# Kernel optimization log

Measured on AMD Instinct MI355X. Metric: run time of the kernel, lower is better.

## Reference

```python
import jax, jax.numpy as jnp
import numpy as np

B, NUM_OBJ, R, D, C = 1024, 128, 32, 512, 7  # scans, obj slots, rel samples, feat dim, rel classes
N = NUM_OBJ + R  # 160 graph nodes per scan


def setup_inputs() -> dict:
    key = jax.random.key(0)
    ks = jax.random.split(key, 8)
    obj_feats = jax.random.normal(ks[0], (B, NUM_OBJ, D), jnp.float32)
    pairs = jax.random.randint(ks[1], (B, R, 2), 0, NUM_OBJ, dtype=jnp.int32)
    init = lambda k, shape, fan_in: jax.random.normal(k, shape, jnp.float32) / np.float32(np.sqrt(fan_in))
    return {
        "obj_feats": obj_feats,
        "pairs": pairs,
        "fuse_w": init(ks[2], (2 * D, D), 2 * D), "fuse_b": jnp.zeros((D,), jnp.float32),
        "gcn_w": init(ks[3], (D, D), D), "gcn_b": jnp.zeros((D,), jnp.float32),
        "fc1_w": init(ks[4], (D, 256), D), "fc1_b": jnp.zeros((256,), jnp.float32),
        "fc2_w": init(ks[5], (256, 128), 256), "fc2_b": jnp.zeros((128,), jnp.float32),
        "fc3_w": init(ks[6], (128, C), 128), "fc3_b": jnp.zeros((C,), jnp.float32),
    }


def reference(obj_feats, pairs, fuse_w, fuse_b, gcn_w, gcn_b,
              fc1_w, fc1_b, fc2_w, fc2_b, fc3_w, fc3_b):
    # --- init_rel_node (pos_fuse=False): fuse sub/obj features per sampled pair ---
    sub = jnp.take_along_axis(obj_feats, pairs[:, :, 0:1], axis=1)  # [B,R,D]
    obj = jnp.take_along_axis(obj_feats, pairs[:, :, 1:2], axis=1)  # [B,R,D]
    init_rel = jnp.concatenate([sub, obj], axis=-1) @ fuse_w + fuse_b  # [B,R,D]

    # --- X: object node feats in rows [0,NUM_OBJ), rel node feats in rows [NUM_OBJ,N) ---
    X = jnp.concatenate([obj_feats, init_rel], axis=1)  # [B,N,D]

    # --- A: get_graph_gcn_with_rel -- scatter 4 directed edges per pair ---
    b_idx = jnp.arange(B)[:, None]                      # [B,1]
    ridx = NUM_OBJ + jnp.arange(R)[None, :]             # [1,R] rel node index j+num_obj
    p0, p1 = pairs[:, :, 0], pairs[:, :, 1]             # [B,R]
    A = jnp.zeros((B, N, N), jnp.float32)
    A = A.at[b_idx, p0, ridx].set(1.0)
    A = A.at[b_idx, ridx, p1].set(1.0)
    A = A.at[b_idx, p1, ridx].set(1.0)
    A = A.at[b_idx, ridx, p0].set(1.0)

    # --- simpleGCN: relu((A @ X) W + b) ---
    H = jax.nn.relu(jnp.einsum('bnm,bmd->bnd', A, X) @ gcn_w + gcn_b)  # [B,N,D]

    # --- residual: GCN rel-node output + init rel feats ---
    rel_feat = H[:, NUM_OBJ:, :] + init_rel  # [B,R,D]

    # --- proxi_detector (dropout = identity, eval behavior) ---
    h = jax.nn.relu(rel_feat @ fc1_w + fc1_b)
    h = jax.nn.relu(h @ fc2_w + fc2_b)
    logits = h @ fc3_w + fc3_b  # [B,R,C]
    return jax.nn.softmax(logits, axis=-1)
```

## Files before the change

### kernel.cpp

```cpp
#include <hip/hip_runtime.h>
#include <hip/hip_bf16.h>

#define B_    1024
#define NOBJ  128
#define RREL  32
#define DIM   512
#define MTOT  32768

typedef __bf16 bf16x8 __attribute__((ext_vector_type(8)));
typedef float  f32x4  __attribute__((ext_vector_type(4)));
typedef unsigned short us;

__device__ __forceinline__ us f2bf(float f) {
    unsigned int u = __float_as_uint(f);
    u += 0x7FFFu + ((u >> 16) & 1u);
    return (us)(u >> 16);
}
__device__ __forceinline__ float bf2f(us h) {
    return __uint_as_float(((unsigned int)h) << 16);
}

__device__ __forceinline__ void load16_to_lds(const us* g, us* l) {
    __builtin_amdgcn_global_load_lds((const __attribute__((address_space(1))) void*)g,
                                     (__attribute__((address_space(3))) void*)l,
                                     16, 0, 0);
}

__global__ __launch_bounds__(256) void gather_kernel(
        const float* __restrict__ obj, const int* __restrict__ pairs,
        us* __restrict__ As, us* __restrict__ Msum) {
    int t = threadIdx.x;
    int g = t >> 7;
    int c = t & 127;
    int base = blockIdx.x * 8;
#pragma unroll
    for (int rr = 0; rr < 4; ++rr) {
        int m  = base + rr * 2 + g;
        int b  = m >> 5;
        int p0 = pairs[(m << 1) + 0];
        int p1 = pairs[(m << 1) + 1];
        const float4* srow = (const float4*)(obj + (size_t)(b * NOBJ + p0) * DIM);
        const float4* orow = (const float4*)(obj + (size_t)(b * NOBJ + p1) * DIM);
        float4 s4 = srow[c];
        float4 o4 = orow[c];
        size_t arow = (size_t)m * 1024;
        ushort4 sb = make_ushort4(f2bf(s4.x), f2bf(s4.y), f2bf(s4.z), f2bf(s4.w));
        ushort4 ob = make_ushort4(f2bf(o4.x), f2bf(o4.y), f2bf(o4.z), f2bf(o4.w));
        *(ushort4*)(As + arow + c * 4)       = sb;
        *(ushort4*)(As + arow + 512 + c * 4) = ob;
        float4 mz = s4;
        if (p0 != p1) { mz.x += o4.x; mz.y += o4.y; mz.z += o4.z; mz.w += o4.w; }
        *(ushort4*)(Msum + (size_t)m * 512 + c * 4) =
            make_ushort4(f2bf(mz.x), f2bf(mz.y), f2bf(mz.z), f2bf(mz.w));
    }
}

__global__ __launch_bounds__(256) void prep_weights(
        const float* __restrict__ fw, const float* __restrict__ gw,
        const float* __restrict__ w1, const float* __restrict__ w2,
        us* __restrict__ WfT, us* __restrict__ WgT,
        us* __restrict__ W1T, us* __restrict__ W2T) {
    __shared__ float t32[32][33];
    int id = blockIdx.x;
    const float* in; us* out; int K, N, local;
    if (id < 512)      { in = fw; out = WfT; K = 1024; N = 512; local = id; }
    else if (id < 768) { in = gw; out = WgT; K = 512;  N = 512; local = id - 512; }
    else if (id < 896) { in = w1; out = W1T; K = 512;  N = 256; local = id - 768; }
    else               { in = w2; out = W2T; K = 256;  N = 128; local = id - 896; }
    int tilesN = N >> 5;
    int bk = (local / tilesN) * 32;
    int bn = (local % tilesN) * 32;
    int t  = threadIdx.x;
    int tx = t & 31, ty = t >> 5;
#pragma unroll
    for (int i = 0; i < 4; ++i)
        t32[ty + i * 8][tx] = in[(size_t)(bk + ty + i * 8) * N + bn + tx];
    __syncthreads();
#pragma unroll
    for (int i = 0; i < 4; ++i)
        out[(size_t)(bn + ty + i * 8) * K + bk + tx] = f2bf(t32[tx][ty + i * 8]);
}

__global__ __launch_bounds__(256, 2) void gemm_fused12(
        const us* __restrict__ As,
        const us* __restrict__ Msum,
        const us* __restrict__ WfT,
        const us* __restrict__ WgT,
        const float* __restrict__ fuse_b, const float* __restrict__ gcn_b,
        us* __restrict__ rf) {
    __shared__ __align__(16) us ldsA[128 * 32];
    __shared__ __align__(16) us ldsB[128 * 32];

    int tid  = threadIdx.x;
    int wid  = tid >> 6;
    int lane = tid & 63;
    int wm   = wid & 1;
    int wn   = wid >> 1;
    int m0   = blockIdx.x * 128;
    int n0   = blockIdx.y * 128;

    f32x4 accF[4][4], accG[4][4];
#pragma unroll
    for (int i = 0; i < 4; ++i)
#pragma unroll
        for (int j = 0; j < 4; ++j)
#pragma unroll
            for (int k = 0; k < 4; ++k) { accF[i][j][k] = 0.0f; accG[i][j][k] = 0.0f; }

    int r = tid >> 2, c = tid & 3;
    us* la0 = ldsA + wid * 512;
    us* la1 = ldsA + 2048 + wid * 512;
    us* lb0 = ldsB + wid * 512;
    us* lb1 = ldsB + 2048 + wid * 512;

    int arow = wm * 64 + (lane & 15);
    int brow = wn * 64 + (lane & 15);
    int koff = (lane >> 4) * 8;

    {
        const us* ag0 = As + (size_t)(m0 + r)      * 1024 + c * 8;
        const us* ag1 = As + (size_t)(m0 + 64 + r) * 1024 + c * 8;
        const us* bg0 = WfT + (size_t)(n0 + r)      * 1024 + c * 8;
        const us* bg1 = WfT + (size_t)(n0 + 64 + r) * 1024 + c * 8;
        for (int k0 = 0; k0 < 1024; k0 += 32) {
            __syncthreads();
            load16_to_lds(ag0 + k0, la0);
            load16_to_lds(ag1 + k0, la1);
            load16_to_lds(bg0 + k0, lb0);
            load16_to_lds(bg1 + k0, lb1);
            __syncthreads();
            bf16x8 a[4], b[4];
#pragma unroll
            for (int i = 0; i < 4; ++i)
                a[i] = *(const bf16x8*)(ldsA + (arow + i * 16) * 32 + koff);
#pragma unroll
            for (int j = 0; j < 4; ++j)
                b[j] = *(const bf16x8*)(ldsB + (brow + j * 16) * 32 + koff);
#pragma unroll
            for (int i = 0; i < 4; ++i)
#pragma unroll
                for (int j = 0; j < 4; ++j)
                    accF[i][j] = __builtin_amdgcn_mfma_f32_16x16x32_bf16(a[i], b[j], accF[i][j], 0, 0, 0);
        }
    }
    {
        const us* ag0 = Msum + (size_t)(m0 + r)      * 512 + c * 8;
        const us* ag1 = Msum + (size_t)(m0 + 64 + r) * 512 + c * 8;
        const us* bg0 = WgT + (size_t)(n0 + r)      * 512 + c * 8;
        const us* bg1 = WgT + (size_t)(n0 + 64 + r) * 512 + c * 8;
        for (int k0 = 0; k0 < 512; k0 += 32) {
            __syncthreads();
            load16_to_lds(ag0 + k0, la0);
            load16_to_lds(ag1 + k0, la1);
            load16_to_lds(bg0 + k0, lb0);
            load16_to_lds(bg1 + k0, lb1);
            __syncthreads();
            bf16x8 a[4], b[4];
#pragma unroll
            for (int i = 0; i < 4; ++i)
                a[i] = *(const bf16x8*)(ldsA + (arow + i * 16) * 32 + koff);
#pragma unroll
            for (int j = 0; j < 4; ++j)
                b[j] = *(const bf16x8*)(ldsB + (brow + j * 16) * 32 + koff);
#pragma unroll
            for (int i = 0; i < 4; ++i)
#pragma unroll
                for (int j = 0; j < 4; ++j)
                    accG[i][j] = __builtin_amdgcn_mfma_f32_16x16x32_bf16(a[i], b[j], accG[i][j], 0, 0, 0);
        }
    }

    int crow  = wm * 64 + (lane >> 4) * 4;
    int ccol0 = wn * 64 + (lane & 15);
    float bf_[4], bg_[4];
#pragma unroll
    for (int j = 0; j < 4; ++j) {
        bf_[j] = fuse_b[n0 + ccol0 + j * 16];
        bg_[j] = gcn_b [n0 + ccol0 + j * 16];
    }
#pragma unroll
    for (int i = 0; i < 4; ++i)
#pragma unroll
        for (int j = 0; j < 4; ++j) {
            int col = n0 + ccol0 + j * 16;
#pragma unroll
            for (int jj = 0; jj < 4; ++jj) {
                int row = m0 + crow + i * 16 + jj;
                float v = fmaxf(accG[i][j][jj] + bg_[j], 0.0f) + accF[i][j][jj] + bf_[j];
                rf[(size_t)row * 512 + col] = f2bf(v);
            }
        }
}

#define H1S 264
#define H2S 136
__global__ __launch_bounds__(256, 2) void tail_kernel(
        const us* __restrict__ rf,
        const us* __restrict__ W1T,
        const us* __restrict__ W2T,
        const float* __restrict__ b1, const float* __restrict__ b2,
        const float* __restrict__ w3, const float* __restrict__ b3,
        float* __restrict__ out) {
    __shared__ __align__(16) unsigned char pool[57888];
    us*    sA   = (us*)(pool);
    us*    sB   = (us*)(pool + 4096);
    us*    sH2  = (us*)(pool);
    us*    sH1  = (us*)(pool + 20480);
    float* sRed = (float*)(pool + 20480);
    float* sW3  = (float*)(pool + 54272);
    float* sB3  = (float*)(pool + 57856);

    int tid  = threadIdx.x;
    int wid  = tid >> 6;
    int lane = tid & 63;
    int m0   = blockIdx.x * 64;

    for (int i = tid; i < 128 * 7; i += 256) sW3[i] = w3[i];
    if (tid < 7) sB3[tid] = b3[tid];

    int r = tid >> 2, c = tid & 3;
    int koff = (lane >> 4) * 8;
    int l15  = lane & 15;

    f32x4 acc1[4][4];
#pragma unroll
    for (int i = 0; i < 4; ++i)
#pragma unroll
        for (int j = 0; j < 4; ++j)
#pragma unroll
            for (int k = 0; k < 4; ++k) acc1[i][j][k] = 0.0f;

    {
        const us* ag = rf + (size_t)(m0 + r) * 512 + c * 8;
        us* la = sA + wid * 512;
        for (int k0 = 0; k0 < 512; k0 += 32) {
            __syncthreads();
            load16_to_lds(ag + k0, la);
#pragma unroll
            for (int q = 0; q < 4; ++q)
                load16_to_lds(W1T + (size_t)(q * 64 + r) * 512 + k0 + c * 8,
                              sB + q * 2048 + wid * 512);
            __syncthreads();
            bf16x8 a[4], b[4];
#pragma unroll
            for (int i = 0; i < 4; ++i)
                a[i] = *(const bf16x8*)(sA + (l15 + i * 16) * 32 + koff);
#pragma unroll
            for (int j = 0; j < 4; ++j)
                b[j] = *(const bf16x8*)(sB + (wid * 64 + j * 16 + l15) * 32 + koff);
#pragma unroll
            for (int i = 0; i < 4; ++i)
#pragma unroll
                for (int j = 0; j < 4; ++j)
                    acc1[i][j] = __builtin_amdgcn_mfma_f32_16x16x32_bf16(a[i], b[j], acc1[i][j], 0, 0, 0);
        }
    }
#pragma unroll
    for (int i = 0; i < 4; ++i)
#pragma unroll
        for (int j = 0; j < 4; ++j) {
            int col = wid * 64 + j * 16 + l15;
            float bb = b1[col];
#pragma unroll
            for (int jj = 0; jj < 4; ++jj) {
                int row = i * 16 + (lane >> 4) * 4 + jj;
                sH1[row * H1S + col] = f2bf(fmaxf(acc1[i][j][jj] + bb, 0.0f));
            }
        }

    int nw = wid & 1, kw = wid >> 1;
    f32x4 acc2[4][4];
#pragma unroll
    for (int i = 0; i < 4; ++i)
#pragma unroll
        for (int j = 0; j < 4; ++j)
#pragma unroll
            for (int k = 0; k < 4; ++k) acc2[i][j][k] = 0.0f;

    for (int t = 0; t < 4; ++t) {
        __syncthreads();
#pragma unroll
        for (int s = 0; s < 2; ++s)
#pragma unroll
            for (int q = 0; q < 2; ++q)
                load16_to_lds(W2T + (size_t)(q * 64 + r) * 256 + s * 128 + t * 32 + c * 8,
                              sB + s * 4096 + q * 2048 + wid * 512);
        __syncthreads();
        bf16x8 a[4], b[4];
#pragma unroll
        for (int i = 0; i < 4; ++i)
            a[i] = *(const bf16x8*)(sH1 + (l15 + i * 16) * H1S + kw * 128 + t * 32 + koff);
#pragma unroll
        for (int j = 0; j < 4; ++j)
            b[j] = *(const bf16x8*)(sB + kw * 4096 + (nw * 64 + j * 16 + l15) * 32 + koff);
#pragma unroll
        for (int i = 0; i < 4; ++i)
#pragma unroll
            for (int j = 0; j < 4; ++j)
                acc2[i][j] = __builtin_amdgcn_mfma_f32_16x16x32_bf16(a[i], b[j], acc2[i][j], 0, 0, 0);
    }
    __syncthreads();
    if (kw == 1) {
#pragma unroll
        for (int i = 0; i < 4; ++i)
#pragma unroll
            for (int j = 0; j < 4; ++j) {
                int col = nw * 64 + j * 16 + l15;
#pragma unroll
                for (int jj = 0; jj < 4; ++jj) {
                    int row = i * 16 + (lane >> 4) * 4 + jj;
                    sRed[row * 132 + col] = acc2[i][j][jj];
                }
            }
    }
    __syncthreads();
    if (kw == 0) {
#pragma unroll
        for (int i = 0; i < 4; ++i)
#pragma unroll
            for (int j = 0; j < 4; ++j) {
                int col = nw * 64 + j * 16 + l15;
                float bb = b2[col];
#pragma unroll
                for (int jj = 0; jj < 4; ++jj) {
                    int row = i * 16 + (lane >> 4) * 4 + jj;
                    float v = acc2[i][j][jj] + sRed[row * 132 + col] + bb;
                    sH2[row * H2S + col] = f2bf(fmaxf(v, 0.0f));
                }
            }
    }
    __syncthreads();

    int row = tid >> 2;
    int p   = tid & 3;
    float accv[7];
#pragma unroll
    for (int cc = 0; cc < 7; ++cc) accv[cc] = 0.0f;
    const us* hrow = sH2 + row * H2S + p * 32;
    for (int kk = 0; kk < 8; ++kk) {
        ushort4 u = *(const ushort4*)(hrow + kk * 4);
        float f0 = bf2f(u.x), f1 = bf2f(u.y), f2 = bf2f(u.z), f3 = bf2f(u.w);
        int k = p * 32 + kk * 4;
#pragma unroll
        for (int cc = 0; cc < 7; ++cc) {
            accv[cc] = fmaf(f0, sW3[(k + 0) * 7 + cc], accv[cc]);
            accv[cc] = fmaf(f1, sW3[(k + 1) * 7 + cc], accv[cc]);
            accv[cc] = fmaf(f2, sW3[(k + 2) * 7 + cc], accv[cc]);
            accv[cc] = fmaf(f3, sW3[(k + 3) * 7 + cc], accv[cc]);
        }
    }
#pragma unroll
    for (int cc = 0; cc < 7; ++cc) {
        accv[cc] += __shfl_xor(accv[cc], 1);
        accv[cc] += __shfl_xor(accv[cc], 2);
    }
    if (p == 0) {
        float mx = accv[0] + sB3[0];
        float lg[7];
#pragma unroll
        for (int cc = 0; cc < 7; ++cc) { lg[cc] = accv[cc] + sB3[cc]; mx = fmaxf(mx, lg[cc]); }
        float sum = 0.f;
#pragma unroll
        for (int cc = 0; cc < 7; ++cc) { lg[cc] = __expf(lg[cc] - mx); sum += lg[cc]; }
        float inv = 1.0f / sum;
#pragma unroll
        for (int cc = 0; cc < 7; ++cc) out[(size_t)(m0 + row) * 7 + cc] = lg[cc] * inv;
    }
}

extern "C" void kernel_launch(void* const* d_in, const int* in_sizes, int n_in,
                              void* d_out, int out_size, void* d_ws, size_t ws_size,
                              hipStream_t stream) {
    (void)in_sizes; (void)n_in; (void)out_size; (void)ws_size;
    const float* obj    = (const float*)d_in[0];
    const int*   pairs  = (const int*)  d_in[1];
    const float* fuse_w = (const float*)d_in[2];
    const float* fuse_b = (const float*)d_in[3];
    const float* gcn_w  = (const float*)d_in[4];
    const float* gcn_b  = (const float*)d_in[5];
    const float* fc1_w  = (const float*)d_in[6];
    const float* fc1_b  = (const float*)d_in[7];
    const float* fc2_w  = (const float*)d_in[8];
    const float* fc2_b  = (const float*)d_in[9];
    const float* fc3_w  = (const float*)d_in[10];
    const float* fc3_b  = (const float*)d_in[11];
    float* out = (float*)d_out;

    char* ws = (char*)d_ws;
    us* As   = (us*)(ws);
    us* Msum = (us*)(ws + (64u  << 20));
    us* rf   = (us*)(ws + (96u  << 20));
    us* WfT  = (us*)(ws + (128u << 20));
    us* WgT  = (us*)(ws + (129u << 20));
    us* W1T  = (us*)(ws + (130u << 20));
    us* W2T  = (us*)(ws + (131u << 20));

    gather_kernel<<<MTOT / 8, 256, 0, stream>>>(obj, pairs, As, Msum);
    prep_weights<<<928, 256, 0, stream>>>(fuse_w, gcn_w, fc1_w, fc2_w,
                                          WfT, WgT, W1T, W2T);

    gemm_fused12<<<dim3(MTOT / 128, 4), 256, 0, stream>>>(
        As, Msum, WfT, WgT, fuse_b, gcn_b, rf);

    tail_kernel<<<MTOT / 64, 256, 0, stream>>>(
        rf, W1T, W2T, fc1_b, fc2_b, fc3_w, fc3_b, out);
}
```

Baseline: 449.6 us.

## Widen fused GEMM to full N with double-buffered LDS and single accumulator

The fused GEMM now uses 512-thread blocks that each cover all 512 output columns for 128 rows, instead of a 4-way grid split over N. This lets the A tile be loaded once per block rather than four times. Global-to-LDS loads are double-buffered, so the next K-slice is staged while MFMAs run on the current one, which cuts the syncs per step to one. The GCN result is computed first, ReLU'd in place, and then the fuse GEMM accumulates into the same registers, so one accumulator set replaces two. The trade-off is 64 KB+ of LDS per block and fewer blocks (256) on a large-CU GPU, which may reduce occupancy and parallelism.

Result: no change. 444.5 us (-1.1%).

```diff
diff --git a/kernel.cpp b/kernel.cpp
--- a/kernel.cpp
+++ b/kernel.cpp
@@ -81,113 +81,114 @@
         out[(size_t)(bn + ty + i * 8) * K + bk + tx] = f2bf(t32[tx][ty + i * 8]);
 }
 
-__global__ __launch_bounds__(256, 2) void gemm_fused12(
+__global__ __launch_bounds__(512, 2) void gemm_fused12(
         const us* __restrict__ As,
         const us* __restrict__ Msum,
         const us* __restrict__ WfT,
         const us* __restrict__ WgT,
         const float* __restrict__ fuse_b, const float* __restrict__ gcn_b,
         us* __restrict__ rf) {
-    __shared__ __align__(16) us ldsA[128 * 32];
-    __shared__ __align__(16) us ldsB[128 * 32];
+    __shared__ __align__(16) us ldsA[2][4096];
+    __shared__ __align__(16) us ldsB[2][16384];
 
     int tid  = threadIdx.x;
     int wid  = tid >> 6;
     int lane = tid & 63;
-    int wm   = wid & 1;
-    int wn   = wid >> 1;
+    int wm   = wid >> 2;
+    int wn   = wid & 3;
     int m0   = blockIdx.x * 128;
-    int n0   = blockIdx.y * 128;
-
-    f32x4 accF[4][4], accG[4][4];
-#pragma unroll
-    for (int i = 0; i < 4; ++i)
-#pragma unroll
-        for (int j = 0; j < 4; ++j)
-#pragma unroll
-            for (int k = 0; k < 4; ++k) { accF[i][j][k] = 0.0f; accG[i][j][k] = 0.0f; }
+
+    f32x4 acc[4][8];
+#pragma unroll
+    for (int i = 0; i < 4; ++i)
+#pragma unroll
+        for (int j = 0; j < 8; ++j)
+#pragma unroll
+            for (int k = 0; k < 4; ++k) acc[i][j][k] = 0.0f;
 
     int r = tid >> 2, c = tid & 3;
-    us* la0 = ldsA + wid * 512;
-    us* la1 = ldsA + 2048 + wid * 512;
-    us* lb0 = ldsB + wid * 512;
-    us* lb1 = ldsB + 2048 + wid * 512;
-
-    int arow = wm * 64 + (lane & 15);
-    int brow = wn * 64 + (lane & 15);
+    const us* aG = Msum + (size_t)(m0 + r) * 512  + c * 8;
+    const us* aF = As   + (size_t)(m0 + r) * 1024 + c * 8;
+
+    int l15  = lane & 15;
     int koff = (lane >> 4) * 8;
-
-    {
-        const us* ag0 = As + (size_t)(m0 + r)      * 1024 + c * 8;
-        const us* ag1 = As + (size_t)(m0 + 64 + r) * 1024 + c * 8;
-        const us* bg0 = WfT + (size_t)(n0 + r)      * 1024 + c * 8;
-        const us* bg1 = WfT + (size_t)(n0 + 64 + r) * 1024 + c * 8;
-        for (int k0 = 0; k0 < 1024; k0 += 32) {
-            __syncthreads();
-            load16_to_lds(ag0 + k0, la0);
-            load16_to_lds(ag1 + k0, la1);
-            load16_to_lds(bg0 + k0, lb0);
-            load16_to_lds(bg1 + k0, lb1);
-            __syncthreads();
-            bf16x8 a[4], b[4];
+    int aoff = (wm * 64  + l15) * 32 + koff;
+    int boff = (wn * 128 + l15) * 32 + koff;
+
+    float bg_[8], bf_[8];
+#pragma unroll
+    for (int j = 0; j < 8; ++j) {
+        int col = wn * 128 + j * 16 + l15;
+        bg_[j] = gcn_b[col];
+        bf_[j] = fuse_b[col];
+    }
+
+    auto stageG = [&](int ks, int buf) {
+        load16_to_lds(aG + ks * 32, &ldsA[buf][tid * 8]);
+#pragma unroll
+        for (int q = 0; q < 4; ++q)
+            load16_to_lds(WgT + (size_t)(q * 128 + r) * 512 + ks * 32 + c * 8,
+                          &ldsB[buf][q * 4096 + tid * 8]);
+    };
+    auto stageF = [&](int ks, int buf) {
+        load16_to_lds(aF + ks * 32, &ldsA[buf][tid * 8]);
+#pragma unroll
+        for (int q = 0; q < 4; ++q)
+            load16_to_lds(WfT + (size_t)(q * 128 + r) * 1024 + ks * 32 + c * 8,
+                          &ldsB[buf][q * 4096 + tid * 8]);
+    };
+    auto compute = [&](int buf) {
+        bf16x8 a[4], b[8];
+#pragma unroll
+        for (int i = 0; i < 4; ++i)
+            a[i] = *(const bf16x8*)(&ldsA[buf][aoff + i * 512]);
+#pragma unroll
+        for (int j = 0; j < 8; ++j)
+            b[j] = *(const bf16x8*)(&ldsB[buf][boff + j * 512]);
+#pragma unroll
+        for (int i = 0; i < 4; ++i)
+#pragma unroll
+            for (int j = 0; j < 8; ++j)
+                acc[i][j] = __builtin_amdgcn_mfma_f32_16x16x32_bf16(a[i], b[j], acc[i][j], 0, 0, 0);
+    };
+
+    int cur = 0;
+    stageG(0, 0);
+    __syncthreads();
+
+    for (int s = 0; s < 16; ++s) {
+        if (s < 15) stageG(s + 1, cur ^ 1);
+        else        stageF(0, cur ^ 1);
+        compute(cur);
+        if (s == 15) {
 #pragma unroll
             for (int i = 0; i < 4; ++i)
-                a[i] = *(const bf16x8*)(ldsA + (arow + i * 16) * 32 + koff);
-#pragma unroll
-            for (int j = 0; j < 4; ++j)
-                b[j] = *(const bf16x8*)(ldsB + (brow + j * 16) * 32 + koff);
-#pragma unroll
-            for (int i = 0; i < 4; ++i)
-#pragma unroll
-                for (int j = 0; j < 4; ++j)
-                    accF[i][j] = __builtin_amdgcn_mfma_f32_16x16x32_bf16(a[i], b[j], accF[i][j], 0, 0, 0);
+#pragma unroll
+                for (int j = 0; j < 8; ++j)
+#pragma unroll
+                    for (int k = 0; k < 4; ++k)
+                        acc[i][j][k] = fmaxf(acc[i][j][k] + bg_[j], 0.0f);
         }
-    }
-    {
-        const us* ag0 = Msum + (size_t)(m0 + r)      * 512 + c * 8;
-        const us* ag1 = Msum + (size_t)(m0 + 64 + r) * 512 + c * 8;
-        const us* bg0 = WgT + (size_t)(n0 + r)      * 512 + c * 8;
-        const us* bg1 = WgT + (size_t)(n0 + 64 + r) * 512 + c * 8;
-        for (int k0 = 0; k0 < 512; k0 += 32) {
-            __syncthreads();
-            load16_to_lds(ag0 + k0, la0);
-            load16_to_lds(ag1 + k0, la1);
-            load16_to_lds(bg0 + k0, lb0);
-            load16_to_lds(bg1 + k0, lb1);
-            __syncthreads();
-            bf16x8 a[4], b[4];
-#pragma unroll
-            for (int i = 0; i < 4; ++i)
-                a[i] = *(const bf16x8*)(ldsA + (arow + i * 16) * 32 + koff);
-#pragma unroll
-            for (int j = 0; j < 4; ++j)
-                b[j] = *(const bf16x8*)(ldsB + (brow + j * 16) * 32 + koff);
-#pragma unroll
-            for (int i = 0; i < 4; ++i)
-#pragma unroll
-                for (int j = 0; j < 4; ++j)
-                    accG[i][j] = __builtin_amdgcn_mfma_f32_16x16x32_bf16(a[i], b[j], accG[i][j], 0, 0, 0);
-        }
-    }
-
-    int crow  = wm * 64 + (lane >> 4) * 4;
-    int ccol0 = wn * 64 + (lane & 15);
-    float bf_[4], bg_[4];
-#pragma unroll
-    for (int j = 0; j < 4; ++j) {
-        bf_[j] = fuse_b[n0 + ccol0 + j * 16];
-        bg_[j] = gcn_b [n0 + ccol0 + j * 16];
-    }
-#pragma unroll
-    for (int i = 0; i < 4; ++i)
-#pragma unroll
-        for (int j = 0; j < 4; ++j) {
-            int col = n0 + ccol0 + j * 16;
+        __syncthreads();
+        cur ^= 1;
+    }
+    for (int s = 0; s < 32; ++s) {
+        if (s < 31) stageF(s + 1, cur ^ 1);
+        compute(cur);
+        __syncthreads();
+        cur ^= 1;
+    }
+
+    int crow = wm * 64 + (lane >> 4) * 4;
+#pragma unroll
+    for (int i = 0; i < 4; ++i)
+#pragma unroll
+        for (int j = 0; j < 8; ++j) {
+            int col = wn * 128 + j * 16 + l15;
 #pragma unroll
             for (int jj = 0; jj < 4; ++jj) {
                 int row = m0 + crow + i * 16 + jj;
-                float v = fmaxf(accG[i][j][jj] + bg_[j], 0.0f) + accF[i][j][jj] + bf_[j];
-                rf[(size_t)row * 512 + col] = f2bf(v);
+                rf[(size_t)row * 512 + col] = f2bf(acc[i][j][jj] + bf_[j]);
             }
         }
 }
@@ -399,7 +400,7 @@
     prep_weights<<<928, 256, 0, stream>>>(fuse_w, gcn_w, fc1_w, fc2_w,
                                           WfT, WgT, W1T, W2T);
 
-    gemm_fused12<<<dim3(MTOT / 128, 4), 256, 0, stream>>>(
+    gemm_fused12<<<MTOT / 128, 512, 0, stream>>>(
         As, Msum, WfT, WgT, fuse_b, gcn_b, rf);
 
     tail_kernel<<<MTOT / 64, 256, 0, stream>>>(
```
